# Kernel optimization log

Measured on AMD Instinct MI355X. Metric: run time of the kernel, lower is better.

Reference implementation:

```python
import jax, jax.numpy as jnp
import numpy as np


def kernel_mus(n_kernels):
    l_mu = [1.0]
    if n_kernels == 1:
        return l_mu
    bin_size = 2.0 / (n_kernels - 1)
    l_mu.append(1 - bin_size / 2)
    for i in range(1, n_kernels - 1):
        l_mu.append(l_mu[i] - bin_size)
    return l_mu


def kernel_sigmas(n_kernels):
    bin_size = 2.0 / (n_kernels - 1)
    l_sigma = [0.0001]
    if n_kernels == 1:
        return l_sigma
    l_sigma += [0.5 * bin_size] * (n_kernels - 1)
    return l_sigma


def setup_inputs() -> dict:
    key = jax.random.key(0)
    k0, k1, k2, k3 = jax.random.split(key, 4)
    B, Q, D, E, V, K = 256, 32, 512, 300, 100000, 11
    query_tokens = jax.random.randint(k0, (B, Q), 0, V)
    doc_tokens = jax.random.randint(k1, (B, D), 0, V)
    emb_table = jax.random.normal(k2, (V, E), jnp.float32) * 0.02
    dense_w = jax.random.uniform(k3, (1, K), jnp.float32, -0.014, 0.014)
    dense_b = jnp.zeros((1,), jnp.float32)
    mu = jnp.asarray(kernel_mus(K), jnp.float32)
    sigma = jnp.asarray(kernel_sigmas(K), jnp.float32)
    return {"query_tokens": query_tokens, "doc_tokens": doc_tokens,
            "emb_table": emb_table, "dense_w": dense_w, "dense_b": dense_b,
            "mu": mu, "sigma": sigma}


def reference(query_tokens, doc_tokens, emb_table, dense_w, dense_b, mu, sigma):
    EPS = 1e-13  # CosineMatrixAttention tiny value
    q_mask = (query_tokens > 0).astype(jnp.float32)   # [B,Q]
    d_mask = (doc_tokens > 0).astype(jnp.float32)     # [B,D]
    q_emb = emb_table[query_tokens]                   # [B,Q,E]
    d_emb = emb_table[doc_tokens]                     # [B,D,E]
    q_n = q_emb / (jnp.linalg.norm(q_emb, axis=-1, keepdims=True) + EPS)
    d_n = d_emb / (jnp.linalg.norm(d_emb, axis=-1, keepdims=True) + EPS)
    cosine = jnp.einsum('bqe,bde->bqd', q_n, d_n)     # [B,Q,D]
    pair_mask = q_mask[:, :, None] * d_mask[:, None, :]  # [B,Q,D]
    cosine_masked = cosine * pair_mask
    # gaussian kernels: [B,Q,D,K]
    diff = cosine_masked[..., None] - mu
    kernels = jnp.exp(-(diff * diff) / (2.0 * sigma * sigma)) * pair_mask[..., None]
    per_kernel_query = jnp.sum(kernels, axis=2)       # [B,Q,K]
    log_pkq = jnp.log(jnp.clip(per_kernel_query, 1e-10)) * 0.01
    log_pkq = log_pkq * q_mask[..., None]
    per_kernel = jnp.sum(log_pkq, axis=1)             # [B,K]
    out = per_kernel @ dense_w.T + dense_b            # [B,1]
    return out[:, 0]
```

## Files before the change

kernel.cpp:

```cpp
#include <hip/hip_runtime.h>


#define B      256
#define BQ     32
#define BD     512
#define EDIM   300
#define KPAD   320
#define NK     11
#define DTILE  32
#define NSEMI  32
#define DSTR   328

typedef float floatx4 __attribute__((ext_vector_type(4)));
typedef short shortx8 __attribute__((ext_vector_type(8)));

__device__ __forceinline__ unsigned short f2bf(float f) {
    unsigned int u = __float_as_uint(f);
    return (unsigned short)((u + 0x7fffu + ((u >> 16) & 1u)) >> 16);
}
__device__ __forceinline__ float bf2f(unsigned short h) {
    return __uint_as_float(((unsigned int)h) << 16);
}

__global__ __launch_bounds__(256)
void knrm_norm(const float* __restrict__ emb, unsigned short* __restrict__ ebf,
               float* __restrict__ rnorm, int V)
{
    int r    = blockIdx.x * 16 + (threadIdx.x >> 4);
    int part = threadIdx.x & 15;
    if (r >= V) return;
    const float4* src = (const float4*)(emb + (size_t)r * EDIM);
    uint2*        dst = (uint2*)(ebf + (size_t)r * KPAD);
    float ss = 0.f;
    #pragma unroll
    for (int i = 0; i < 5; ++i) {
        int c = part + i * 16;
        uint2 p = {0u, 0u};
        if (c < EDIM / 4) {
            float4 v = src[c];
            unsigned short h0 = f2bf(v.x), h1 = f2bf(v.y), h2 = f2bf(v.z), h3 = f2bf(v.w);
            p.x = (unsigned int)h0 | ((unsigned int)h1 << 16);
            p.y = (unsigned int)h2 | ((unsigned int)h3 << 16);
            float f0 = bf2f(h0), f1 = bf2f(h1), f2 = bf2f(h2), f3 = bf2f(h3);
            ss += f0 * f0 + f1 * f1 + f2 * f2 + f3 * f3;
        }
        dst[c] = p;
    }
    ss += __shfl_xor(ss, 1);
    ss += __shfl_xor(ss, 2);
    ss += __shfl_xor(ss, 4);
    ss += __shfl_xor(ss, 8);
    if (part == 0) rnorm[r] = 1.f / (sqrtf(ss) + 1e-13f);
}

__global__ __launch_bounds__(256, 5)
void knrm_main4(const int* __restrict__ qtok, const int* __restrict__ dtok,
                const unsigned short* __restrict__ ebf, const float* __restrict__ rnorm,
                const float* __restrict__ mu, const float* __restrict__ sigma,
                float* __restrict__ pkq_part)
{
    __shared__ unsigned short d_buf[DTILE * DSTR];

    const int tid   = threadIdx.x;
    const int lane  = tid & 63;
    const int wv    = tid >> 6;
    const int b     = blockIdx.x & 255;
    const int chunk = blockIdx.x >> 8;
    const int l16   = lane & 15;
    const int quad  = lane >> 4;
    const int mbase = (wv & 1) * 16;
    const int nbase = (wv >> 1) * 16;
    const int dbase = chunk * DTILE;

    const int tq = qtok[b * BQ + mbase + l16];
    const int td = dtok[b * BD + dbase + nbase + l16];
    float rq = rnorm[tq];
    float rd = rnorm[td];
    float dm = (td > 0) ? 1.f : 0.f;

    const uint4* asrc = (const uint4*)(ebf + (size_t)tq * KPAD);
    shortx8 afrag[10];
    #pragma unroll
    for (int ks = 0; ks < 10; ++ks)
        afrag[ks] = *(const shortx8*)&asrc[quad + ks * 4];

    float mur[NK], cfr[NK];
    #pragma unroll
    for (int k = 0; k < NK; ++k) {
        float s = sigma[k];
        mur[k] = mu[k];
        cfr[k] = -0.5f / (s * s);
    }

    {
        int row = tid >> 3, part = tid & 7;
        int tok = dtok[b * BD + dbase + row];
        const uint4* src = (const uint4*)(ebf + (size_t)tok * KPAD);
        #pragma unroll
        for (int i = 0; i < 5; ++i) {
            int c = part + i * 8;
            *(uint4*)&d_buf[row * DSTR + c * 8] = src[c];
        }
    }
    __syncthreads();

    const unsigned short* bptr = &d_buf[(nbase + l16) * DSTR + quad * 8];
    floatx4 acc = {0.f, 0.f, 0.f, 0.f};
    #pragma unroll
    for (int ks = 0; ks < 10; ++ks) {
        shortx8 bf = *(const shortx8*)(bptr + ks * 32);
        acc = __builtin_amdgcn_mfma_f32_16x16x32_bf16(afrag[ks], bf, acc, 0, 0, 0);
    }

    float rqv[4];
    #pragma unroll
    for (int r = 0; r < 4; ++r) rqv[r] = __shfl(rq, quad * 4 + r);

    const int semi = chunk * 2 + (nbase >> 4);
    float* dst = pkq_part + (size_t)(b * NSEMI + semi) * (BQ * NK);
    #pragma unroll
    for (int r = 0; r < 4; ++r) {
        float c0 = acc[r] * rqv[r] * rd;
        int q = mbase + quad * 4 + r;
        #pragma unroll
        for (int k = 0; k < NK; ++k) {
            float d0 = c0 - mur[k];
            float v = dm * __expf(cfr[k] * d0 * d0);
            v += __shfl_xor(v, 1);
            v += __shfl_xor(v, 2);
            v += __shfl_xor(v, 4);
            v += __shfl_xor(v, 8);
            if (l16 == 0) dst[q * NK + k] = v;
        }
    }
}

__global__ __launch_bounds__(64)
void knrm_epi(const int* __restrict__ qtok, const float* __restrict__ dw,
              const float* __restrict__ db, const float* __restrict__ pkq_part,
              float* __restrict__ out)
{
    int b = blockIdx.x, lane = threadIdx.x;
    float sq = 0.f;
    if (lane < BQ) {
        int tok = qtok[b * BQ + lane];
        if (tok > 0) {
            #pragma unroll
            for (int k = 0; k < NK; ++k) {
                float s = 0.f;
                #pragma unroll
                for (int c = 0; c < NSEMI; ++c)
                    s += pkq_part[((size_t)(b * NSEMI + c) * BQ + lane) * NK + k];
                sq += __logf(fmaxf(s, 1e-10f)) * 0.01f * dw[k];
            }
        }
    }
    sq += __shfl_xor(sq, 1);
    sq += __shfl_xor(sq, 2);
    sq += __shfl_xor(sq, 4);
    sq += __shfl_xor(sq, 8);
    sq += __shfl_xor(sq, 16);
    sq += __shfl_xor(sq, 32);
    if (lane == 0) out[b] = sq + db[0];
}

extern "C" void kernel_launch(void* const* d_in, const int* in_sizes, int n_in,
                              void* d_out, int out_size, void* d_ws, size_t ws_size,
                              hipStream_t stream)
{
    const int*   qtok  = (const int*)d_in[0];
    const int*   dtok  = (const int*)d_in[1];
    const float* emb   = (const float*)d_in[2];
    const float* dw    = (const float*)d_in[3];
    const float* dbias = (const float*)d_in[4];
    const float* mu    = (const float*)d_in[5];
    const float* sg    = (const float*)d_in[6];
    float* out = (float*)d_out;

    const int V = in_sizes[2] / EDIM;
    const size_t ebf_bytes = (size_t)V * KPAD * 2;
    const size_t rn_bytes  = (size_t)V * 4;

    unsigned short* ebf = (unsigned short*)d_ws;
    float* rnorm        = (float*)((char*)d_ws + ebf_bytes);
    float* pkq_part     = (float*)((char*)d_ws + ebf_bytes + rn_bytes);

    knrm_norm<<<(V + 15) / 16, 256, 0, stream>>>(emb, ebf, rnorm, V);
    knrm_main4<<<B * 16, 256, 0, stream>>>(qtok, dtok, ebf, rnorm, mu, sg, pkq_part);
    knrm_epi<<<B, 64, 0, stream>>>(qtok, dw, dbias, pkq_part, out);
}
```

Before: 247.3 us.

## Stage query embeddings in LDS and widen doc tile per block

```diff
diff --git a/kernel.cpp b/kernel.cpp
--- a/kernel.cpp
+++ b/kernel.cpp
@@ -7,9 +7,8 @@
 #define EDIM   300
 #define KPAD   320
 #define NK     11
-#define DTILE  32
 #define NSEMI  32
-#define DSTR   328
+#define QSTR   328
 
 typedef float floatx4 __attribute__((ext_vector_type(4)));
 typedef short shortx8 __attribute__((ext_vector_type(8)));
@@ -20,6 +19,9 @@
 }
 __device__ __forceinline__ float bf2f(unsigned short h) {
     return __uint_as_float(((unsigned int)h) << 16);
+}
+__device__ __forceinline__ float sbc(float x) {
+    return __uint_as_float(__builtin_amdgcn_readfirstlane(__float_as_uint(x)));
 }
 
 __global__ __launch_bounds__(256)
@@ -54,83 +56,87 @@
 }
 
 __global__ __launch_bounds__(256, 5)
-void knrm_main4(const int* __restrict__ qtok, const int* __restrict__ dtok,
+void knrm_main5(const int* __restrict__ qtok, const int* __restrict__ dtok,
                 const unsigned short* __restrict__ ebf, const float* __restrict__ rnorm,
                 const float* __restrict__ mu, const float* __restrict__ sigma,
                 float* __restrict__ pkq_part)
 {
-    __shared__ unsigned short d_buf[DTILE * DSTR];
+    __shared__ unsigned short q_buf[BQ * QSTR];
+    __shared__ float rqs[BQ];
 
-    const int tid   = threadIdx.x;
-    const int lane  = tid & 63;
-    const int wv    = tid >> 6;
-    const int b     = blockIdx.x & 255;
-    const int chunk = blockIdx.x >> 8;
-    const int l16   = lane & 15;
-    const int quad  = lane >> 4;
-    const int mbase = (wv & 1) * 16;
-    const int nbase = (wv >> 1) * 16;
-    const int dbase = chunk * DTILE;
+    const int tid  = threadIdx.x;
+    const int lane = tid & 63;
+    const int wv   = tid >> 6;
+    const int b    = blockIdx.x & 255;
+    const int g    = blockIdx.x >> 8;
+    const int l16  = lane & 15;
+    const int quad = lane >> 4;
 
-    const int tq = qtok[b * BQ + mbase + l16];
-    const int td = dtok[b * BD + dbase + nbase + l16];
-    float rq = rnorm[tq];
-    float rd = rnorm[td];
-    float dm = (td > 0) ? 1.f : 0.f;
+    const int td = dtok[b * BD + g * 64 + wv * 16 + l16];
+    const float rd = rnorm[td];
+    const float dm = (td > 0) ? 1.f : 0.f;
 
-    const uint4* asrc = (const uint4*)(ebf + (size_t)tq * KPAD);
-    shortx8 afrag[10];
+    const uint4* bsrc = (const uint4*)(ebf + (size_t)td * KPAD);
+    shortx8 bfrag[10];
     #pragma unroll
     for (int ks = 0; ks < 10; ++ks)
-        afrag[ks] = *(const shortx8*)&asrc[quad + ks * 4];
+        bfrag[ks] = *(const shortx8*)&bsrc[quad + ks * 4];
+
+    if (tid < BQ) rqs[tid] = rnorm[qtok[b * BQ + tid]];
+
+    {
+        int row = tid >> 3, part = tid & 7;
+        int tok = qtok[b * BQ + row];
+        const uint4* src = (const uint4*)(ebf + (size_t)tok * KPAD);
+        #pragma unroll
+        for (int i = 0; i < 5; ++i) {
+            int c = part + i * 8;
+            *(uint4*)&q_buf[row * QSTR + c * 8] = src[c];
+        }
+    }
+    __syncthreads();
 
     float mur[NK], cfr[NK];
     #pragma unroll
     for (int k = 0; k < NK; ++k) {
-        float s = sigma[k];
-        mur[k] = mu[k];
+        float s = sbc(sigma[k]);
+        mur[k] = sbc(mu[k]);
         cfr[k] = -0.5f / (s * s);
     }
 
-    {
-        int row = tid >> 3, part = tid & 7;
-        int tok = dtok[b * BD + dbase + row];
-        const uint4* src = (const uint4*)(ebf + (size_t)tok * KPAD);
-        #pragma unroll
-        for (int i = 0; i < 5; ++i) {
-            int c = part + i * 8;
-            *(uint4*)&d_buf[row * DSTR + c * 8] = src[c];
-        }
-    }
-    __syncthreads();
+    const unsigned short* a0 = &q_buf[l16 * QSTR + quad * 8];
+    const unsigned short* a1 = a0 + 16 * QSTR;
 
-    const unsigned short* bptr = &d_buf[(nbase + l16) * DSTR + quad * 8];
-    floatx4 acc = {0.f, 0.f, 0.f, 0.f};
+    floatx4 acc0 = {0.f, 0.f, 0.f, 0.f};
+    floatx4 acc1 = {0.f, 0.f, 0.f, 0.f};
     #pragma unroll
     for (int ks = 0; ks < 10; ++ks) {
-        shortx8 bf = *(const shortx8*)(bptr + ks * 32);
-        acc = __builtin_amdgcn_mfma_f32_16x16x32_bf16(afrag[ks], bf, acc, 0, 0, 0);
+        shortx8 aA = *(const shortx8*)(a0 + ks * 32);
+        shortx8 aB = *(const shortx8*)(a1 + ks * 32);
+        acc0 = __builtin_amdgcn_mfma_f32_16x16x32_bf16(aA, bfrag[ks], acc0, 0, 0, 0);
+        acc1 = __builtin_amdgcn_mfma_f32_16x16x32_bf16(aB, bfrag[ks], acc1, 0, 0, 0);
     }
 
-    float rqv[4];
+    const int semi = g * 4 + wv;
+    float* dst = pkq_part + (size_t)(b * NSEMI + semi) * (BQ * NK);
+
     #pragma unroll
-    for (int r = 0; r < 4; ++r) rqv[r] = __shfl(rq, quad * 4 + r);
-
-    const int semi = chunk * 2 + (nbase >> 4);
-    float* dst = pkq_part + (size_t)(b * NSEMI + semi) * (BQ * NK);
-    #pragma unroll
-    for (int r = 0; r < 4; ++r) {
-        float c0 = acc[r] * rqv[r] * rd;
-        int q = mbase + quad * 4 + r;
+    for (int slab = 0; slab < 2; ++slab) {
+        floatx4 acc = slab ? acc1 : acc0;
         #pragma unroll
-        for (int k = 0; k < NK; ++k) {
-            float d0 = c0 - mur[k];
-            float v = dm * __expf(cfr[k] * d0 * d0);
-            v += __shfl_xor(v, 1);
-            v += __shfl_xor(v, 2);
-            v += __shfl_xor(v, 4);
-            v += __shfl_xor(v, 8);
-            if (l16 == 0) dst[q * NK + k] = v;
+        for (int r = 0; r < 4; ++r) {
+            int q = slab * 16 + quad * 4 + r;
+            float c0 = acc[r] * rqs[q] * rd;
+            #pragma unroll
+            for (int k = 0; k < NK; ++k) {
+                float d0 = c0 - mur[k];
+                float v = dm * __expf(cfr[k] * d0 * d0);
+                v += __shfl_xor(v, 1);
+                v += __shfl_xor(v, 2);
+                v += __shfl_xor(v, 4);
+                v += __shfl_xor(v, 8);
+                if (l16 == 0) dst[q * NK + k] = v;
+            }
         }
     }
 }
@@ -186,6 +192,6 @@
     float* pkq_part     = (float*)((char*)d_ws + ebf_bytes + rn_bytes);
 
     knrm_norm<<<(V + 15) / 16, 256, 0, stream>>>(emb, ebf, rnorm, V);
-    knrm_main4<<<B * 16, 256, 0, stream>>>(qtok, dtok, ebf, rnorm, mu, sg, pkq_part);
+    knrm_main5<<<B * 8, 256, 0, stream>>>(qtok, dtok, ebf, rnorm, mu, sg, pkq_part);
     knrm_epi<<<B, 64, 0, stream>>>(qtok, dw, dbias, pkq_part, out);
 }
```

New measurement: 248.5 us. About the same (+0.5%).
